# Performance work log

Measured on AMD Instinct MI355X. Metric: run time of the kernel, lower is better.

## Reference

```python
import jax, jax.numpy as jnp
import numpy as np

B = 65536
G = 9          # grid_size
C = 10         # num_classes
BS = 3         # block_size = sqrt(grid_size)
CONSTRAINT_WEIGHT = 0.1


def setup_inputs() -> dict:
    key = jax.random.key(0)
    k1, k2, k3 = jax.random.split(key, 3)
    logits = jax.random.normal(k1, (B, G, G, C), dtype=jnp.float32)
    targets = jax.random.randint(k2, (B, G, G), 0, C)
    puzzles = jax.random.randint(k3, (B, G, G), 0, C)
    return {"logits": logits, "targets": targets, "puzzles": puzzles}


def _sudoku_loss(logits, targets, puzzles):
    mask = (puzzles == 0).astype(logits.dtype)               # [B, G, G]

    # --- masked cross-entropy over empty cells ---
    logp = jax.nn.log_softmax(logits, axis=-1)               # [B, G, G, C]
    ce = -jnp.take_along_axis(logp, targets[..., None], axis=-1)[..., 0]
    ce_loss = (ce * mask).sum() / (mask.sum() + 1e-8)

    # --- constraint loss (rows, cols, 3x3 boxes), fully vectorized ---
    probs = jnp.exp(logp)                                    # softmax probs
    wp = probs * mask[..., None]                             # [B, G, G, C]

    def group_mse(digit_sums, msum):
        # digit_sums: [B, G_groups, C]; msum: [B, G_groups]
        # torch: per-group F.mse_loss over [B, C-1], summed over groups
        target = msum[..., None] / G                         # [B, Gg, 1]
        diff = digit_sums[..., 1:] - target                  # [B, Gg, C-1]
        return (diff * diff).mean(axis=(0, 2)).sum()

    # rows: sum over columns (axis 2)
    row_loss = group_mse(wp.sum(axis=2), mask.sum(axis=2))
    # cols: sum over rows (axis 1)
    col_loss = group_mse(wp.sum(axis=1), mask.sum(axis=1))
    # boxes: reshape to [B, bi, ri, bj, cj, C], sum within-box dims
    box_ds = wp.reshape(B, BS, BS, BS, BS, C).sum(axis=(2, 4)).reshape(B, G, C)
    box_ms = mask.reshape(B, BS, BS, BS, BS).sum(axis=(2, 4)).reshape(B, G)
    box_loss = group_mse(box_ds, box_ms)

    num_constraints = G * 2 + BS * BS                        # 27
    constraint_loss = (row_loss + col_loss + box_loss) / num_constraints

    # torch wraps the constraint loss in torch.tensor(...), detaching it
    total = ce_loss + CONSTRAINT_WEIGHT * jax.lax.stop_gradient(constraint_loss)
    return total, ce_loss, constraint_loss


def reference(logits, targets, puzzles):
    total, ce_loss, constraint_loss = _sudoku_loss(logits, targets, puzzles)
    return total, ce_loss, constraint_loss
```

## Files before the change

### kernel.cpp

```cpp
#include <hip/hip_runtime.h>


constexpr int kB = 65536;

__global__ __launch_bounds__(192) void sudoku_main(
    const float* __restrict__ logits,
    const int*   __restrict__ targets,
    const int*   __restrict__ puzzles,
    float*       __restrict__ ws)
{
    __shared__ float colacc[64 * 90];
    __shared__ float red[3][3];

    const int tid = threadIdx.x;
    for (int i = tid; i < 64 * 90; i += 192) colacc[i] = 0.f;
    __syncthreads();

    const int gt = blockIdx.x * 192 + tid;
    const int p  = gt / 3;
    const int k  = gt % 3;
    const int q  = tid / 3;

    const float* lg  = logits  + (size_t)p * 810 + (size_t)k * 270;
    const int*   tgp = targets + (size_t)p * 81  + k * 27;
    const int*   pzp = puzzles + (size_t)p * 81  + k * 27;

    int pzv[27];
    #pragma unroll
    for (int i = 0; i < 27; ++i) pzv[i] = pzp[i];

    float boxsum[3][9];
    float boxm[3] = {0.f, 0.f, 0.f};
    #pragma unroll
    for (int b = 0; b < 3; ++b)
        #pragma unroll
        for (int c = 0; c < 9; ++c) boxsum[b][c] = 0.f;

    float diff2 = 0.f, ce = 0.f, mcnt = 0.f;
    float* mycol = &colacc[q * 90];

    #pragma unroll
    for (int r = 0; r < 3; ++r) {
        float rowsum[9];
        #pragma unroll
        for (int c = 0; c < 9; ++c) rowsum[c] = 0.f;
        float rowm = 0.f;

        #pragma unroll
        for (int j = 0; j < 9; ++j) {
            const int cell = r * 9 + j;
            if (pzv[cell] == 0) {
                const float* xp = lg + cell * 10;
                float x[10];
                #pragma unroll
                for (int h = 0; h < 5; ++h) {
                    const float2 v = *(const float2*)(xp + 2 * h);
                    x[2 * h] = v.x; x[2 * h + 1] = v.y;
                }
                float mx = x[0];
                #pragma unroll
                for (int c = 1; c < 10; ++c) mx = fmaxf(mx, x[c]);
                float e[10];
                float S = 0.f;
                #pragma unroll
                for (int c = 0; c < 10; ++c) { e[c] = __expf(x[c] - mx); S += e[c]; }
                const float inv = 1.0f / S;
                const float lse = __logf(S);

                const int t = tgp[cell];
                float xt = x[0];
                #pragma unroll
                for (int c = 1; c < 10; ++c) xt = (t == c) ? x[c] : xt;
                ce   += mx + lse - xt;
                mcnt += 1.f;
                rowm += 1.f;
                const int jb = j / 3;
                boxm[jb] += 1.f;
                atomicAdd(&mycol[j * 10 + 9], 1.f);
                #pragma unroll
                for (int c = 1; c < 10; ++c) {
                    const float w = e[c] * inv;
                    rowsum[c - 1]     += w;
                    boxsum[jb][c - 1] += w;
                    atomicAdd(&mycol[j * 10 + (c - 1)], w);
                }
            }
        }
        const float tr = rowm * (1.f / 9.f);
        #pragma unroll
        for (int c = 0; c < 9; ++c) { const float d = rowsum[c] - tr; diff2 += d * d; }
    }
    #pragma unroll
    for (int b = 0; b < 3; ++b) {
        const float tb = boxm[b] * (1.f / 9.f);
        #pragma unroll
        for (int c = 0; c < 9; ++c) { const float d = boxsum[b][c] - tb; diff2 += d * d; }
    }

    __syncthreads();
    #pragma unroll
    for (int jj = 0; jj < 3; ++jj) {
        const int j = 3 * k + jj;
        const float tc = mycol[j * 10 + 9] * (1.f / 9.f);
        #pragma unroll
        for (int c = 0; c < 9; ++c) {
            const float d = mycol[j * 10 + c] - tc;
            diff2 += d * d;
        }
    }

    #pragma unroll
    for (int off = 32; off > 0; off >>= 1) {
        diff2 += __shfl_down(diff2, off);
        ce    += __shfl_down(ce, off);
        mcnt  += __shfl_down(mcnt, off);
    }
    const int wave = tid >> 6;
    if ((tid & 63) == 0) { red[0][wave] = diff2; red[1][wave] = ce; red[2][wave] = mcnt; }
    __syncthreads();
    if (tid == 0) {
        const float d  = red[0][0] + red[0][1] + red[0][2];
        const float c2 = red[1][0] + red[1][1] + red[1][2];
        const float m  = red[2][0] + red[2][1] + red[2][2];
        atomicAdd(&ws[0], d);
        atomicAdd(&ws[1], c2);
        atomicAdd(&ws[2], m);
    }
}

__global__ void sudoku_final(const float* __restrict__ ws, float* __restrict__ out)
{
    const float diff2   = ws[0];
    const float ce_sum  = ws[1];
    const float msum    = ws[2];
    const float ce_loss = ce_sum / (msum + 1e-8f);
    const float constraint = diff2 / ((float)kB * 9.f * 27.f);
    out[0] = ce_loss + 0.1f * constraint;
    out[1] = ce_loss;
    out[2] = constraint;
}

extern "C" void kernel_launch(void* const* d_in, const int* in_sizes, int n_in,
                              void* d_out, int out_size, void* d_ws, size_t ws_size,
                              hipStream_t stream)
{
    const float* logits  = (const float*)d_in[0];
    const int*   targets = (const int*)d_in[1];
    const int*   puzzles = (const int*)d_in[2];
    float* ws  = (float*)d_ws;
    float* out = (float*)d_out;

    hipMemsetAsync(d_ws, 0, 3 * sizeof(float), stream);

    const int blocks = (kB * 3) / 192;
    sudoku_main<<<blocks, 192, 0, stream>>>(logits, targets, puzzles, ws);
    sudoku_final<<<1, 1, 0, stream>>>(ws, out);
}
```

Baseline: 326.4 us.

## Map one thread per sudoku row and replace global atomics with per-block partials

Restructures work so each thread handles one row of a puzzle, with 7 puzzles per wave and 4 waves per block, and computes box sums through lane shuffles. Softmax now runs on every cell and is masked branchlessly instead of skipping empty cells. Global atomics and the memset are replaced by per-block partial sums that a 256-thread final kernel reduces. The per-thread loads become more uniform and the global atomic contention goes away, at the cost of 1 idle lane per wave, extra softmax work on filled cells, and a larger final reduction.

```diff
diff --git a/kernel.cpp b/kernel.cpp
--- a/kernel.cpp
+++ b/kernel.cpp
@@ -2,142 +2,184 @@
 
 
 constexpr int kB = 65536;
+constexpr int kPuzzPerWave  = 7;
+constexpr int kWavesPerBlk  = 4;
+constexpr int kPuzzPerBlk   = kPuzzPerWave * kWavesPerBlk;
+constexpr int kBlocks       = (kB + kPuzzPerBlk - 1) / kPuzzPerBlk;
 
-__global__ __launch_bounds__(192) void sudoku_main(
+__global__ __launch_bounds__(256) void sudoku_main(
     const float* __restrict__ logits,
     const int*   __restrict__ targets,
     const int*   __restrict__ puzzles,
     float*       __restrict__ ws)
 {
-    __shared__ float colacc[64 * 90];
-    __shared__ float red[3][3];
+    __shared__ float colacc[kPuzzPerBlk * 90];
+    __shared__ float red[kWavesPerBlk][3];
 
     const int tid = threadIdx.x;
-    for (int i = tid; i < 64 * 90; i += 192) colacc[i] = 0.f;
+    #pragma unroll
+    for (int i = tid; i < kPuzzPerBlk * 90; i += 256) colacc[i] = 0.f;
     __syncthreads();
 
-    const int gt = blockIdx.x * 192 + tid;
-    const int p  = gt / 3;
-    const int k  = gt % 3;
-    const int q  = tid / 3;
+    const int wave = tid >> 6;
+    const int lane = tid & 63;
+    const int plw  = lane / 9;
+    const int r    = lane - plw * 9;
+    const int pLoc = wave * kPuzzPerWave + plw;
+    const int p    = blockIdx.x * kPuzzPerBlk + pLoc;
 
-    const float* lg  = logits  + (size_t)p * 810 + (size_t)k * 270;
-    const int*   tgp = targets + (size_t)p * 81  + k * 27;
-    const int*   pzp = puzzles + (size_t)p * 81  + k * 27;
+    const bool active = (plw < kPuzzPerWave) && (p < kB);
 
-    int pzv[27];
+    float ce = 0.f, rowm = 0.f, diff2 = 0.f;
+    float rowsum[9];
+    float boxp[3][9];
+    float bm[3] = {0.f, 0.f, 0.f};
     #pragma unroll
-    for (int i = 0; i < 27; ++i) pzv[i] = pzp[i];
-
-    float boxsum[3][9];
-    float boxm[3] = {0.f, 0.f, 0.f};
+    for (int c = 0; c < 9; ++c) rowsum[c] = 0.f;
     #pragma unroll
     for (int b = 0; b < 3; ++b)
         #pragma unroll
-        for (int c = 0; c < 9; ++c) boxsum[b][c] = 0.f;
+        for (int c = 0; c < 9; ++c) boxp[b][c] = 0.f;
 
-    float diff2 = 0.f, ce = 0.f, mcnt = 0.f;
-    float* mycol = &colacc[q * 90];
+    if (active) {
+        const float* lg = logits  + (size_t)p * 810 + r * 90;
+        const int*   tg = targets + (size_t)p * 81  + r * 9;
+        const int*   pz = puzzles + (size_t)p * 81  + r * 9;
 
-    #pragma unroll
-    for (int r = 0; r < 3; ++r) {
-        float rowsum[9];
+        int pzv[9], tgv[9];
         #pragma unroll
-        for (int c = 0; c < 9; ++c) rowsum[c] = 0.f;
-        float rowm = 0.f;
+        for (int j = 0; j < 9; ++j) pzv[j] = pz[j];
+        #pragma unroll
+        for (int j = 0; j < 9; ++j) tgv[j] = tg[j];
+
+        float* colrow = &colacc[pLoc * 90];
 
         #pragma unroll
         for (int j = 0; j < 9; ++j) {
-            const int cell = r * 9 + j;
-            if (pzv[cell] == 0) {
-                const float* xp = lg + cell * 10;
-                float x[10];
+            const float* xp = lg + j * 10;
+            float x[10];
+            #pragma unroll
+            for (int h = 0; h < 5; ++h) {
+                const float2 v = *(const float2*)(xp + 2 * h);
+                x[2 * h] = v.x; x[2 * h + 1] = v.y;
+            }
+            float mx = x[0];
+            #pragma unroll
+            for (int c = 1; c < 10; ++c) mx = fmaxf(mx, x[c]);
+            float e[10], S = 0.f;
+            #pragma unroll
+            for (int c = 0; c < 10; ++c) { e[c] = __expf(x[c] - mx); S += e[c]; }
+            const float inv = 1.f / S;
+            const float lse = __logf(S);
+
+            const int t = tgv[j];
+            float xt = x[0];
+            #pragma unroll
+            for (int c = 1; c < 10; ++c) xt = (t == c) ? x[c] : xt;
+
+            const float maskf = (pzv[j] == 0) ? 1.f : 0.f;
+            ce   += maskf * (mx + lse - xt);
+            rowm += maskf;
+            const int jb = j / 3;
+            bm[jb] += maskf;
+
+            const float winv = inv * maskf;
+            float w[9];
+            #pragma unroll
+            for (int c = 1; c < 10; ++c) {
+                w[c - 1] = e[c] * winv;
+                rowsum[c - 1]   += w[c - 1];
+                boxp[jb][c - 1] += w[c - 1];
+            }
+            if (pzv[j] == 0) {
+                float* cb = colrow + j * 10;
+                atomicAdd(&cb[0], 1.f);
                 #pragma unroll
-                for (int h = 0; h < 5; ++h) {
-                    const float2 v = *(const float2*)(xp + 2 * h);
-                    x[2 * h] = v.x; x[2 * h + 1] = v.y;
-                }
-                float mx = x[0];
-                #pragma unroll
-                for (int c = 1; c < 10; ++c) mx = fmaxf(mx, x[c]);
-                float e[10];
-                float S = 0.f;
-                #pragma unroll
-                for (int c = 0; c < 10; ++c) { e[c] = __expf(x[c] - mx); S += e[c]; }
-                const float inv = 1.0f / S;
-                const float lse = __logf(S);
-
-                const int t = tgp[cell];
-                float xt = x[0];
-                #pragma unroll
-                for (int c = 1; c < 10; ++c) xt = (t == c) ? x[c] : xt;
-                ce   += mx + lse - xt;
-                mcnt += 1.f;
-                rowm += 1.f;
-                const int jb = j / 3;
-                boxm[jb] += 1.f;
-                atomicAdd(&mycol[j * 10 + 9], 1.f);
-                #pragma unroll
-                for (int c = 1; c < 10; ++c) {
-                    const float w = e[c] * inv;
-                    rowsum[c - 1]     += w;
-                    boxsum[jb][c - 1] += w;
-                    atomicAdd(&mycol[j * 10 + (c - 1)], w);
-                }
+                for (int c = 1; c < 10; ++c) atomicAdd(&cb[c], w[c - 1]);
             }
         }
+
         const float tr = rowm * (1.f / 9.f);
         #pragma unroll
         for (int c = 0; c < 9; ++c) { const float d = rowsum[c] - tr; diff2 += d * d; }
-    }
-    #pragma unroll
-    for (int b = 0; b < 3; ++b) {
-        const float tb = boxm[b] * (1.f / 9.f);
+
+        const bool boxLead = (r == 0) || (r == 3) || (r == 6);
         #pragma unroll
-        for (int c = 0; c < 9; ++c) { const float d = boxsum[b][c] - tb; diff2 += d * d; }
+        for (int bj = 0; bj < 3; ++bj) {
+            float bmm = bm[bj];
+            bmm += __shfl_down(bm[bj], 1);
+            bmm += __shfl_down(bm[bj], 2);
+            const float tb = bmm * (1.f / 9.f);
+            #pragma unroll
+            for (int c = 0; c < 9; ++c) {
+                float bs = boxp[bj][c];
+                bs += __shfl_down(boxp[bj][c], 1);
+                bs += __shfl_down(boxp[bj][c], 2);
+                const float d = bs - tb;
+                diff2 += boxLead ? d * d : 0.f;
+            }
+        }
     }
 
     __syncthreads();
-    #pragma unroll
-    for (int jj = 0; jj < 3; ++jj) {
-        const int j = 3 * k + jj;
-        const float tc = mycol[j * 10 + 9] * (1.f / 9.f);
+
+    if (active) {
+        const float* cb = &colacc[pLoc * 90 + r * 10];
+        const float tc = cb[0] * (1.f / 9.f);
         #pragma unroll
-        for (int c = 0; c < 9; ++c) {
-            const float d = mycol[j * 10 + c] - tc;
-            diff2 += d * d;
-        }
+        for (int c = 1; c < 10; ++c) { const float d = cb[c] - tc; diff2 += d * d; }
     }
 
     #pragma unroll
     for (int off = 32; off > 0; off >>= 1) {
         diff2 += __shfl_down(diff2, off);
         ce    += __shfl_down(ce, off);
-        mcnt  += __shfl_down(mcnt, off);
+        rowm  += __shfl_down(rowm, off);
     }
-    const int wave = tid >> 6;
-    if ((tid & 63) == 0) { red[0][wave] = diff2; red[1][wave] = ce; red[2][wave] = mcnt; }
+    if (lane == 0) { red[wave][0] = diff2; red[wave][1] = ce; red[wave][2] = rowm; }
     __syncthreads();
     if (tid == 0) {
-        const float d  = red[0][0] + red[0][1] + red[0][2];
-        const float c2 = red[1][0] + red[1][1] + red[1][2];
-        const float m  = red[2][0] + red[2][1] + red[2][2];
-        atomicAdd(&ws[0], d);
-        atomicAdd(&ws[1], c2);
-        atomicAdd(&ws[2], m);
+        float d = 0.f, c2 = 0.f, m = 0.f;
+        #pragma unroll
+        for (int wv = 0; wv < kWavesPerBlk; ++wv) {
+            d += red[wv][0]; c2 += red[wv][1]; m += red[wv][2];
+        }
+        const int b = blockIdx.x;
+        ws[b]               = d;
+        ws[kBlocks + b]     = c2;
+        ws[2 * kBlocks + b] = m;
     }
 }
 
-__global__ void sudoku_final(const float* __restrict__ ws, float* __restrict__ out)
+__global__ __launch_bounds__(256) void sudoku_final(
+    const float* __restrict__ ws, float* __restrict__ out)
 {
-    const float diff2   = ws[0];
-    const float ce_sum  = ws[1];
-    const float msum    = ws[2];
-    const float ce_loss = ce_sum / (msum + 1e-8f);
-    const float constraint = diff2 / ((float)kB * 9.f * 27.f);
-    out[0] = ce_loss + 0.1f * constraint;
-    out[1] = ce_loss;
-    out[2] = constraint;
+    __shared__ float red[4][3];
+    float s0 = 0.f, s1 = 0.f, s2 = 0.f;
+    for (int i = threadIdx.x; i < kBlocks; i += 256) {
+        s0 += ws[i];
+        s1 += ws[kBlocks + i];
+        s2 += ws[2 * kBlocks + i];
+    }
+    #pragma unroll
+    for (int off = 32; off > 0; off >>= 1) {
+        s0 += __shfl_down(s0, off);
+        s1 += __shfl_down(s1, off);
+        s2 += __shfl_down(s2, off);
+    }
+    const int wave = threadIdx.x >> 6;
+    if ((threadIdx.x & 63) == 0) { red[wave][0] = s0; red[wave][1] = s1; red[wave][2] = s2; }
+    __syncthreads();
+    if (threadIdx.x == 0) {
+        float d = 0.f, c2 = 0.f, m = 0.f;
+        #pragma unroll
+        for (int wv = 0; wv < 4; ++wv) { d += red[wv][0]; c2 += red[wv][1]; m += red[wv][2]; }
+        const float ce_loss    = c2 / (m + 1e-8f);
+        const float constraint = d / ((float)kB * 9.f * 27.f);
+        out[0] = ce_loss + 0.1f * constraint;
+        out[1] = ce_loss;
+        out[2] = constraint;
+    }
 }
 
 extern "C" void kernel_launch(void* const* d_in, const int* in_sizes, int n_in,
@@ -150,9 +192,6 @@
     float* ws  = (float*)d_ws;
     float* out = (float*)d_out;
 
-    hipMemsetAsync(d_ws, 0, 3 * sizeof(float), stream);
-
-    const int blocks = (kB * 3) / 192;
-    sudoku_main<<<blocks, 192, 0, stream>>>(logits, targets, puzzles, ws);
-    sudoku_final<<<1, 1, 0, stream>>>(ws, out);
+    sudoku_main<<<kBlocks, 256, 0, stream>>>(logits, targets, puzzles, ws);
+    sudoku_final<<<1, 256, 0, stream>>>(ws, out);
 }
```

Result: slower. 361.9 us (+10.9%).
